# Kernel tuning notes

Hardware: AMD Instinct MI355X
Metric: run time of the kernel (lower is better)

## Reference

```python
import jax, jax.numpy as jnp
import numpy as np

N_E, N_R, E = 100000, 1000, 1000000
E_HID, R_HID = 128, 128
NEG_SLOPE = 0.01


def _seg_softmax(logits, seg, num_segments):
    # torch_geometric.utils.softmax: per-segment max-subtracted softmax, +1e-16 in denom
    m = jax.ops.segment_max(logits, seg, num_segments=num_segments)
    m = jnp.where(jnp.isfinite(m), m, 0.0)  # empty segments
    z = jnp.exp(logits - m[seg])
    s = jax.ops.segment_sum(z, seg, num_segments=num_segments)
    return z / (s[seg] + 1e-16)


def setup_inputs() -> dict:
    key = jax.random.key(0)
    ks = jax.random.split(key, 10)
    s_e = 1.0 / np.sqrt(E_HID)
    s_r = 1.0 / np.sqrt(R_HID)
    s_2r = 1.0 / np.sqrt(2 * R_HID)
    return {
        "x_e": jax.random.normal(ks[0], (N_E, E_HID), jnp.float32),
        "x_r": jax.random.normal(ks[1], (N_R, R_HID), jnp.float32),
        "edge_index": jax.random.randint(ks[2], (2, E), 0, N_E, jnp.int32),
        "rel": jax.random.randint(ks[3], (E,), 0, N_R, jnp.int32),
        "rel_all": jax.random.randint(ks[4], (N_R,), 0, N_R, jnp.int32),
        "w_ah": jax.random.uniform(ks[5], (E_HID,), jnp.float32, -s_e, s_e),
        "w_at": jax.random.uniform(ks[6], (E_HID,), jnp.float32, -s_e, s_e),
        "w_ar": jax.random.uniform(ks[7], (R_HID,), jnp.float32, -s_r, s_r),
        "W_r1": jax.random.uniform(ks[8], (R_HID, 2 * R_HID), jnp.float32, -s_r, s_r),
        "b_r1": jnp.zeros((2 * R_HID,), jnp.float32),
        "W_r2": jax.random.uniform(ks[9], (2 * R_HID, R_HID), jnp.float32, -s_2r, s_2r),
        "b_r2": jnp.zeros((R_HID,), jnp.float32),
        "W_r": jax.random.uniform(jax.random.fold_in(key, 99), (2 * R_HID, 2 * R_HID), jnp.float32, -s_2r, s_2r),
        "b_r": jnp.zeros((2 * R_HID,), jnp.float32),
    }


def reference(x_e, x_r, edge_index, rel, rel_all, w_ah, w_at, w_ar,
              W_r1, b_r1, W_r2, b_r2, W_r, b_r):
    h, t = edge_index[0], edge_index[1]
    n_e = x_e.shape[0]

    # per-node/per-rel attention scores, gathered per edge
    e_h = (x_e @ w_ah)[h]          # [E]
    e_t = (x_e @ w_at)[t]          # [E]
    e_r = (x_r @ w_ar)[rel]        # [E]

    alpha_h = _seg_softmax(jax.nn.leaky_relu(e_h + e_r, NEG_SLOPE), h, n_e)
    alpha_t = _seg_softmax(jax.nn.leaky_relu(e_t + e_r, NEG_SLOPE), t, n_e)

    # relation transform (no activation in original)
    x_r2 = (x_r @ W_r1 + b_r1) @ W_r2 + b_r2   # [N_r, r_hidden]
    msg = x_r + x_r2                            # [N_r, r_hidden]

    # sparse.mm(adj, msg) == weighted scatter-add over edges
    msg_e = msg[rel]                            # [E, r_hidden]
    x_e_h = jax.ops.segment_sum(alpha_h[:, None] * msg_e, h, num_segments=n_e)
    x_e_t = jax.ops.segment_sum(alpha_t[:, None] * msg_e, t, num_segments=n_e)

    x = jnp.concatenate([x_e_h, x_e_t], axis=1)  # [N_e, 2*r_hidden]
    return x @ W_r + b_r
```

## Files before the change

kernel.cpp:

```cpp
#include <hip/hip_runtime.h>
#include <hip/hip_fp16.h>


#define CH1    2048
#define SUPW   4096
#define CAP1   45056
#define CH2    4096
#define CHUNK2 (CAP1 / CH2)
#define NBPS   128
#define CAP2   512
#define MAXD   64
#define NSB    2048

#define MIX_LO(acc, w, z) \
    asm("v_fma_mix_f32 %0, %1, %2, %0 op_sel:[0,0,0] op_sel_hi:[1,0,0]" \
        : "+v"(acc) : "v"(w), "v"(z))
#define MIX_HI(acc, w, z) \
    asm("v_fma_mix_f32 %0, %1, %2, %0 op_sel:[1,0,0] op_sel_hi:[1,0,0]" \
        : "+v"(acc) : "v"(w), "v"(z))

__device__ __forceinline__ float dot4(float4 a, float4 b) {
    return a.x * b.x + a.y * b.y + a.z * b.z + a.w * b.w;
}

__global__ __launch_bounds__(256) void k_front(
    const float* __restrict__ xe, const float* __restrict__ xr,
    const float* __restrict__ wah, const float* __restrict__ wat, const float* __restrict__ war,
    const float* __restrict__ W1, const float* __restrict__ b1,
    const float* __restrict__ W2, const float* __restrict__ b2,
    const float* __restrict__ Wr,
    const int* __restrict__ ei,
    float* __restrict__ eh, float* __restrict__ et, float* __restrict__ er,
    __half* __restrict__ Mh, __half* __restrict__ Mt,
    int* __restrict__ hist,
    int nE, int nR, int E, int nH, int nSR) {
    __shared__ float xs[128];
    __shared__ float hs[256];
    __shared__ float ms[128];
    __shared__ int cnt[64];
    int b = blockIdx.x, tid = threadIdx.x;
    int lane = tid & 63;
    if (b < nR) {
        int r = b, j = tid;
        if (j < 128) xs[j] = xr[(size_t)r * 128 + j];
        __syncthreads();
        {
            float acc = b1[j];
            #pragma unroll 4
            for (int k = 0; k < 128; ++k) acc += xs[k] * W1[k * 256 + j];
            hs[j] = acc;
        }
        __syncthreads();
        if (j < 128) {
            float acc = b2[j] + xs[j];
            #pragma unroll 4
            for (int k = 0; k < 256; ++k) acc += hs[k] * W2[k * 128 + j];
            ms[j] = acc;
        }
        __syncthreads();
        {
            float ah = 0.f, at_ = 0.f;
            #pragma unroll 4
            for (int i = 0; i < 128; ++i) {
                float m = ms[i];
                ah  += m * Wr[i * 256 + j];
                at_ += m * Wr[(128 + i) * 256 + j];
            }
            Mh[(size_t)r * 256 + j] = __float2half(ah);
            Mt[(size_t)r * 256 + j] = __float2half(at_);
        }
    } else if (b < nR + nH) {
        int blk = b - nR;
        if (tid < 64) cnt[tid] = 0;
        __syncthreads();
        int base = blk * CH1;
        #pragma unroll
        for (int k = 0; k < CH1 / 256; ++k) {
            int e = base + k * 256 + tid;
            if (e < E) {
                unsigned vh = ((unsigned)ei[e]) << 1;
                unsigned vt = (((unsigned)ei[E + e]) << 1) | 1u;
                atomicAdd(&cnt[vh >> 12], 1);
                atomicAdd(&cnt[vt >> 12], 1);
            }
        }
        __syncthreads();
        if (tid < 64) hist[tid * 512 + blk] = cnt[tid];
    } else if (b < nR + nH + nSR) {
        int row = (b - nR - nH) * 32 + (tid >> 6) * 8 + (lane >> 3);
        int seg = lane & 7;
        if (row < nR) {
            const float4* xp = (const float4*)(xr + (size_t)row * 128 + seg * 16);
            const float4* cp = (const float4*)(war + seg * 16);
            float d = 0.f;
            #pragma unroll
            for (int q = 0; q < 4; ++q) d += dot4(xp[q], cp[q]);
            #pragma unroll
            for (int m = 4; m >= 1; m >>= 1) d += __shfl_xor(d, m);
            if (seg == 0) er[row] = d;
        }
    } else {
        int sb = b - nR - nH - nSR;
        int rowInTile = (tid >> 6) * 8 + (lane >> 3);
        int seg = lane & 7;
        const float4* ap = (const float4*)(wah + seg * 16);
        const float4* bp = (const float4*)(wat + seg * 16);
        float4 a0 = ap[0], a1 = ap[1], a2 = ap[2], a3 = ap[3];
        float4 b0 = bp[0], b1_ = bp[1], b2_ = bp[2], b3 = bp[3];
        int row0 = sb * 32 + rowInTile;
        int row1 = row0 + NSB * 32;
        int r1c = min(row1, nE - 1);
        const float4* p0 = (const float4*)(xe + (size_t)row0 * 128 + seg * 16);
        const float4* p1 = (const float4*)(xe + (size_t)r1c * 128 + seg * 16);
        float4 u0 = p0[0], u1 = p0[1], u2 = p0[2], u3 = p0[3];
        float4 w0 = p1[0], w1 = p1[1], w2 = p1[2], w3 = p1[3];
        float dh0 = dot4(u0, a0) + dot4(u1, a1) + dot4(u2, a2) + dot4(u3, a3);
        float dt0 = dot4(u0, b0) + dot4(u1, b1_) + dot4(u2, b2_) + dot4(u3, b3);
        float dh1 = dot4(w0, a0) + dot4(w1, a1) + dot4(w2, a2) + dot4(w3, a3);
        float dt1 = dot4(w0, b0) + dot4(w1, b1_) + dot4(w2, b2_) + dot4(w3, b3);
        #pragma unroll
        for (int m = 4; m >= 1; m >>= 1) {
            dh0 += __shfl_xor(dh0, m); dt0 += __shfl_xor(dt0, m);
            dh1 += __shfl_xor(dh1, m); dt1 += __shfl_xor(dt1, m);
        }
        if (seg == 0) {
            eh[row0] = dh0; et[row0] = dt0;
            if (row1 < nE) { eh[row1] = dh1; et[row1] = dt1; }
        }
    }
}

__global__ __launch_bounds__(256) void k_scanp(
    int* __restrict__ hist, int* __restrict__ bcur1,
    int* __restrict__ bcur2, int nbuck, int nblk) {
    __shared__ int wtot[4];
    int bin = blockIdx.x, tid = threadIdx.x, lane = tid & 63, wid = tid >> 6;
    for (int g = bin * 256 + tid; g < nbuck; g += 64 * 256) bcur2[g] = 0;
    int j0 = 2 * tid, j1 = 2 * tid + 1;
    int v0 = (j0 < nblk) ? hist[bin * 512 + j0] : 0;
    int v1 = (j1 < nblk) ? hist[bin * 512 + j1] : 0;
    int ts = v0 + v1;
    int incl = ts;
    #pragma unroll
    for (int d = 1; d < 64; d <<= 1) { int u = __shfl_up(incl, d); if (lane >= d) incl += u; }
    if (lane == 63) wtot[wid] = incl;
    __syncthreads();
    int wbase = 0;
    for (int w = 0; w < wid; ++w) wbase += wtot[w];
    int excl = wbase + incl - ts;
    hist[bin * 512 + j0] = excl;
    hist[bin * 512 + j1] = excl + v0;
    if (tid == 255) bcur1[bin] = wbase + incl;
}

__global__ __launch_bounds__(256) void k_part1(
    const int* __restrict__ ei, const int* __restrict__ rel,
    const int* __restrict__ hist, unsigned* __restrict__ part1, int E) {
    __shared__ unsigned stage[CH1 * 2];
    __shared__ int cnt[64], offs_[64], cur[64], gb[64];
    int tid = threadIdx.x;
    if (tid < 64) cnt[tid] = 0;
    __syncthreads();
    int base = blockIdx.x * CH1;
    unsigned wh[CH1 / 256], wt[CH1 / 256];
    bool ve[CH1 / 256];
    #pragma unroll
    for (int k = 0; k < CH1 / 256; ++k) {
        int e = base + k * 256 + tid;
        ve[k] = (e < E);
        unsigned h = 0, t = 0, r = 0;
        if (ve[k]) { h = (unsigned)ei[e]; t = (unsigned)ei[E + e]; r = (unsigned)rel[e]; }
        unsigned vh = h << 1, vt = (t << 1) | 1u;
        wh[k] = ((vh >> 12) << 26) | ((vh & 4095u) << 10) | r;
        wt[k] = ((vt >> 12) << 26) | ((vt & 4095u) << 10) | r;
        if (ve[k]) { atomicAdd(&cnt[wh[k] >> 26], 1); atomicAdd(&cnt[wt[k] >> 26], 1); }
    }
    __syncthreads();
    if (tid < 64) {
        int v = cnt[tid], incl = v;
        #pragma unroll
        for (int d = 1; d < 64; d <<= 1) { int u = __shfl_up(incl, d); if (tid >= d) incl += u; }
        offs_[tid] = incl - v;
        cur[tid] = incl - v;
        gb[tid] = hist[tid * 512 + blockIdx.x];
    }
    __syncthreads();
    #pragma unroll
    for (int k = 0; k < CH1 / 256; ++k) {
        if (ve[k]) {
            int p = atomicAdd(&cur[wh[k] >> 26], 1); stage[p] = wh[k];
            int q = atomicAdd(&cur[wt[k] >> 26], 1); stage[q] = wt[k];
        }
    }
    __syncthreads();
    int total = offs_[63] + cnt[63];
    for (int p = tid; p < total; p += 256) {
        unsigned w = stage[p];
        int bin = w >> 26;
        int dst = gb[bin] + (p - offs_[bin]);
        if (dst < CAP1) part1[(size_t)bin * CAP1 + dst] = w & 0x03FFFFFFu;
    }
}

__global__ __launch_bounds__(256) void k_part2(
    const int* __restrict__ bcur1, const unsigned* __restrict__ part1,
    int* __restrict__ bcur2, unsigned short* __restrict__ part2) {
    int s = blockIdx.x / CHUNK2, c = blockIdx.x % CHUNK2;
    int cnt_s = min(bcur1[s], CAP1);
    int start = c * CH2;
    if (start >= cnt_s) return;
    __shared__ unsigned stage[CH2];
    __shared__ int cnt[NBPS], offs_[NBPS], cur[NBPS], gb[NBPS];
    __shared__ int wt2[2];
    int tid = threadIdx.x;
    if (tid < NBPS) cnt[tid] = 0;
    __syncthreads();
    unsigned w_[CH2 / 256];
    bool v_[CH2 / 256];
    #pragma unroll
    for (int k = 0; k < CH2 / 256; ++k) {
        int i = start + k * 256 + tid;
        v_[k] = (i < cnt_s);
        unsigned it = v_[k] ? part1[(size_t)s * CAP1 + i] : 0u;
        unsigned sb = ((it >> 10) & 4095u) >> 5;
        unsigned entry = (((it >> 10) & 31u) << 10) | (it & 1023u);
        w_[k] = (sb << 16) | entry;
        if (v_[k]) atomicAdd(&cnt[sb], 1);
    }
    __syncthreads();
    int v128 = 0, incl128 = 0;
    if (tid < NBPS) {
        v128 = cnt[tid]; incl128 = v128;
        int lane = tid & 63;
        #pragma unroll
        for (int d = 1; d < 64; d <<= 1) { int u = __shfl_up(incl128, d); if (lane >= d) incl128 += u; }
        if (lane == 63) wt2[tid >> 6] = incl128;
    }
    __syncthreads();
    if (tid < NBPS) {
        int base2 = (tid >= 64) ? wt2[0] : 0;
        int excl = base2 + incl128 - v128;
        offs_[tid] = excl;
        cur[tid] = excl;
        gb[tid] = atomicAdd(&bcur2[s * NBPS + tid], v128);
    }
    __syncthreads();
    #pragma unroll
    for (int k = 0; k < CH2 / 256; ++k)
        if (v_[k]) { int p = atomicAdd(&cur[w_[k] >> 16], 1); stage[p] = w_[k]; }
    __syncthreads();
    int total = offs_[NBPS - 1] + cnt[NBPS - 1];
    for (int p = tid; p < total; p += 256) {
        unsigned w = stage[p];
        int sb = w >> 16;
        int dst = gb[sb] + (p - offs_[sb]);
        if (dst < CAP2) part2[((size_t)s * NBPS + sb) * CAP2 + dst] = (unsigned short)w;
    }
}

__global__ __launch_bounds__(256) void k_group_out10(
    const int* __restrict__ bcur2, const unsigned short* __restrict__ part2,
    const float* __restrict__ eh, const float* __restrict__ et, const float* __restrict__ er,
    const __half* __restrict__ Mh, const __half* __restrict__ Mt,
    const float* __restrict__ br, float* __restrict__ out, int nE, int nR) {
    __shared__ unsigned short csr[CAP2];
    __shared__ float er_s[1024];
    __shared__ unsigned zbufZ[4][2][64];
    __shared__ unsigned zbufO[4][2][64];
    __shared__ int cnt[32], offs_[32], cur[32];
    int b = blockIdx.x, tid = threadIdx.x;
    int count = min(bcur2[b], CAP2);
    unsigned mtOff = (unsigned)nR * 512u;
    if (tid < 32) cnt[tid] = 0;
    for (int i = tid; i < nR; i += 256) er_s[i] = er[i];
    __syncthreads();
    unsigned short ev[CAP2 / 256];
    bool val[CAP2 / 256];
    #pragma unroll
    for (int k = 0; k < CAP2 / 256; ++k) {
        int i = tid + k * 256;
        val[k] = (i < count);
        ev[k] = val[k] ? part2[(size_t)b * CAP2 + i] : (unsigned short)0;
        if (val[k]) atomicAdd(&cnt[ev[k] >> 10], 1);
    }
    __syncthreads();
    if (tid < 32) {
        int v = cnt[tid], incl = v;
        #pragma unroll
        for (int d = 1; d < 32; d <<= 1) { int u = __shfl_up(incl, d); if (tid >= d) incl += u; }
        offs_[tid] = incl - v;
        cur[tid] = incl - v;
    }
    __syncthreads();
    #pragma unroll
    for (int k = 0; k < CAP2 / 256; ++k) {
        if (val[k]) {
            int p = atomicAdd(&cur[ev[k] >> 10], 1);
            csr[p] = (unsigned short)(ev[k] & 1023u);
        }
    }
    __syncthreads();
    int lane = tid & 63, wid = tid >> 6;
    int half = lane >> 5, l31 = lane & 31;
    unsigned loff = (unsigned)(l31 << 4);
    const char* Mbase = (const char*)Mh;
    float4 bv = *(const float4*)(br + l31 * 8 + half * 4);
    int nbase = b * 16;
    for (int li = wid; li < 16; li += 4) {
        int n = nbase + li;
        if (n >= nE) break;
        int oH = offs_[2 * li];
        int oT = offs_[2 * li + 1];
        int dH = min(cur[2 * li] - oH, MAXD);
        int dT = min(cur[2 * li + 1] - oT, MAXD);
        float ehn = eh[n], etn = et[n];
        unsigned zHv = 0u, oHv = 0u;
        unsigned zTv = 0u, oTv = mtOff;
        if (lane < dH) {
            int r = csr[oH + lane];
            float l = ehn + er_s[r]; l = l > 0.f ? l : 0.01f * l;
            zHv = __float_as_uint(__expf(l)) & 0xFFFFFC00u;
            oHv = (unsigned)r << 9;
        }
        if (lane < dT) {
            int r = csr[oT + lane];
            float l = etn + er_s[r]; l = l > 0.f ? l : 0.01f * l;
            zTv = __float_as_uint(__expf(l)) & 0xFFFFFC00u;
            oTv = ((unsigned)r << 9) + mtOff;
        }
        zbufZ[wid][0][lane] = zHv; zbufO[wid][0][lane] = oHv;
        zbufZ[wid][1][lane] = zTv; zbufO[wid][1][lane] = oTv;
        const unsigned* zrowZ = &zbufZ[wid][half][0];
        const unsigned* zrowO = &zbufO[wid][half][0];
        float acc[8] = {0, 0, 0, 0, 0, 0, 0, 0};
        float s = 0.f;
        int kk = (max(dH, dT) + 3) & ~3;
        for (int j = 0; j < kk; j += 4) {
            uint4 z4 = *(const uint4*)(zrowZ + j);
            uint4 o4 = *(const uint4*)(zrowO + j);
            unsigned za[4] = {z4.x, z4.y, z4.z, z4.w};
            unsigned oa[4] = {o4.x, o4.y, o4.z, o4.w};
            #pragma unroll
            for (int i = 0; i < 4; ++i) {
                float z = __uint_as_float(za[i]);
                uint4 m = *(const uint4*)(Mbase + (oa[i] + loff));
                MIX_LO(acc[0], m.x, z); MIX_HI(acc[1], m.x, z);
                MIX_LO(acc[2], m.y, z); MIX_HI(acc[3], m.y, z);
                MIX_LO(acc[4], m.z, z); MIX_HI(acc[5], m.z, z);
                MIX_LO(acc[6], m.w, z); MIX_HI(acc[7], m.w, z);
                s += z;
            }
        }
        float sO = __shfl_xor(s, 32);
        float iMine = 1.f / (s + 1e-16f);
        float iOther = 1.f / (sO + 1e-16f);
        float oq[4];
        #pragma unroll
        for (int q = 0; q < 4; ++q) {
            float send = half ? acc[q] : acc[4 + q];
            float mine = half ? acc[4 + q] : acc[q];
            float recv = __shfl_xor(send, 32);
            oq[q] = mine * iMine + recv * iOther;
        }
        float4 o;
        o.x = oq[0] + bv.x;
        o.y = oq[1] + bv.y;
        o.z = oq[2] + bv.z;
        o.w = oq[3] + bv.w;
        *(float4*)(out + (size_t)n * 256 + l31 * 8 + half * 4) = o;
    }
}

__global__ __launch_bounds__(256) void k_scores(
    const float* __restrict__ xe, const float* __restrict__ xr,
    const float* __restrict__ wah, const float* __restrict__ wat, const float* __restrict__ war,
    float* __restrict__ eh, float* __restrict__ et, float* __restrict__ er,
    int nE, int nR) {
    int wid = (blockIdx.x * blockDim.x + threadIdx.x) >> 6;
    int lane = threadIdx.x & 63;
    if (wid < nE) {
        float2 x2 = *(const float2*)(xe + (size_t)wid * 128 + lane * 2);
        float2 a2 = *(const float2*)(wah + lane * 2);
        float2 b2 = *(const float2*)(wat + lane * 2);
        float dh = x2.x * a2.x + x2.y * a2.y;
        float dt = x2.x * b2.x + x2.y * b2.y;
        #pragma unroll
        for (int m = 32; m >= 1; m >>= 1) { dh += __shfl_xor(dh, m); dt += __shfl_xor(dt, m); }
        if (lane == 0) { eh[wid] = dh; et[wid] = dt; }
    } else if (wid < nE + nR) {
        int r = wid - nE;
        float2 x2 = *(const float2*)(xr + (size_t)r * 128 + lane * 2);
        float2 c2 = *(const float2*)(war + lane * 2);
        float d = x2.x * c2.x + x2.y * c2.y;
        #pragma unroll
        for (int m = 32; m >= 1; m >>= 1) d += __shfl_xor(d, m);
        if (lane == 0) er[r] = d;
    }
}

__global__ __launch_bounds__(256) void k_rel(
    const float* __restrict__ xr,
    const float* __restrict__ W1, const float* __restrict__ b1,
    const float* __restrict__ W2, const float* __restrict__ b2,
    const float* __restrict__ Wr,
    __half* __restrict__ Mh, __half* __restrict__ Mt) {
    __shared__ float xs[128];
    __shared__ float hs[256];
    __shared__ float ms[128];
    int r = blockIdx.x, j = threadIdx.x;
    if (j < 128) xs[j] = xr[(size_t)r * 128 + j];
    __syncthreads();
    {
        float acc = b1[j];
        #pragma unroll 4
        for (int k = 0; k < 128; ++k) acc += xs[k] * W1[k * 256 + j];
        hs[j] = acc;
    }
    __syncthreads();
    if (j < 128) {
        float acc = b2[j] + xs[j];
        #pragma unroll 4
        for (int k = 0; k < 256; ++k) acc += hs[k] * W2[k * 128 + j];
        ms[j] = acc;
    }
    __syncthreads();
    {
        float ah = 0.f, at_ = 0.f;
        #pragma unroll 4
        for (int i = 0; i < 128; ++i) {
            float m = ms[i];
            ah  += m * Wr[i * 256 + j];
            at_ += m * Wr[(128 + i) * 256 + j];
        }
        Mh[(size_t)r * 256 + j] = __float2half(ah);
        Mt[(size_t)r * 256 + j] = __float2half(at_);
    }
}

__global__ __launch_bounds__(256) void k_hist(
    const int* __restrict__ ei, int* __restrict__ deg, int E, int nE) {
    int e = blockIdx.x * blockDim.x + threadIdx.x;
    if (e >= E) return;
    atomicAdd(&deg[ei[e]], 1);
    atomicAdd(&deg[nE + ei[E + e]], 1);
}

__global__ __launch_bounds__(256) void k_scan1(
    const int* __restrict__ deg, int* __restrict__ offs, int* __restrict__ bsum, int N) {
    __shared__ int wtot[4];
    int tid = threadIdx.x, lane = tid & 63, wid = tid >> 6;
    int base = blockIdx.x * 1024 + tid * 4;
    int v[4];
    #pragma unroll
    for (int i = 0; i < 4; ++i) v[i] = (base + i < N) ? deg[base + i] : 0;
    int ts = v[0] + v[1] + v[2] + v[3];
    int incl = ts;
    #pragma unroll
    for (int d = 1; d < 64; d <<= 1) { int u = __shfl_up(incl, d); if (lane >= d) incl += u; }
    if (lane == 63) wtot[wid] = incl;
    __syncthreads();
    int wbase = 0;
    for (int w = 0; w < wid; ++w) wbase += wtot[w];
    int run = wbase + incl - ts;
    #pragma unroll
    for (int i = 0; i < 4; ++i) { if (base + i < N) offs[base + i] = run; run += v[i]; }
    if (tid == 255) bsum[blockIdx.x] = wbase + incl;
}

__global__ __launch_bounds__(256) void k_scan2(int* __restrict__ bsum, int NB) {
    __shared__ int wtot[4];
    int tid = threadIdx.x, lane = tid & 63, wid = tid >> 6;
    int v = (tid < NB) ? bsum[tid] : 0;
    int incl = v;
    #pragma unroll
    for (int d = 1; d < 64; d <<= 1) { int u = __shfl_up(incl, d); if (lane >= d) incl += u; }
    if (lane == 63) wtot[wid] = incl;
    __syncthreads();
    int wbase = 0;
    for (int w = 0; w < wid; ++w) wbase += wtot[w];
    if (tid < NB) bsum[tid] = wbase + incl - v;
}

__global__ __launch_bounds__(256) void k_scan3(
    int* __restrict__ offs, const int* __restrict__ bsum, int* __restrict__ cursor, int N) {
    int i = blockIdx.x * blockDim.x + threadIdx.x;
    if (i >= N) return;
    int v = offs[i] + bsum[i >> 10];
    offs[i] = v;
    cursor[i] = v;
}

__global__ __launch_bounds__(256) void k_scatter_offs(
    const int* __restrict__ ei, const int* __restrict__ rel,
    const float* __restrict__ eh, const float* __restrict__ et, const float* __restrict__ er,
    int* __restrict__ cursor, unsigned* __restrict__ csr, int E, int nE) {
    int e = blockIdx.x * blockDim.x + threadIdx.x;
    if (e >= E) return;
    int h = ei[e], t = ei[E + e], r = rel[e];
    float erv = er[r];
    float lh = eh[h] + erv; lh = lh > 0.f ? lh : 0.01f * lh;
    float lt = et[t] + erv; lt = lt > 0.f ? lt : 0.01f * lt;
    unsigned zh = (__float_as_uint(__expf(lh)) & 0xFFFFFC00u) | (unsigned)r;
    unsigned zt = (__float_as_uint(__expf(lt)) & 0xFFFFFC00u) | (unsigned)r;
    int ph = atomicAdd(&cursor[h], 1);
    csr[ph] = zh;
    int pt = atomicAdd(&cursor[nE + t], 1);
    csr[pt] = zt;
}

__global__ __launch_bounds__(256) void k_out_offs(
    const int* __restrict__ offs, const int* __restrict__ deg, const unsigned* __restrict__ csr,
    const __half* __restrict__ Mh, const __half* __restrict__ Mt, const float* __restrict__ br,
    float* __restrict__ out, int nE) {
    int wid = (blockIdx.x * blockDim.x + threadIdx.x) >> 6;
    int lane = threadIdx.x & 63;
    if (wid >= nE) return;
    int dH = deg[wid], dT = deg[nE + wid];
    size_t offH = (size_t)offs[wid], offT = (size_t)offs[nE + wid];
    float4 accH = {0, 0, 0, 0}, accT = {0, 0, 0, 0};
    float sH = 0.f, sT = 0.f;
    int dM = max(dH, dT);
    for (int b = 0; b < dM; b += 64) {
        int kH = min(64, dH - b);
        int kT = min(64, dT - b);
        unsigned eH = 0, eT = 0;
        if (lane < kH) eH = csr[offH + b + lane];
        if (lane < kT) eT = csr[offT + b + lane];
        int kk = max(kH, kT);
        for (int j = 0; j < kk; ++j) {
            unsigned cH = (unsigned)__shfl((int)eH, j);
            unsigned cT = (unsigned)__shfl((int)eT, j);
            if (j < kH) {
                float z = __uint_as_float(cH & 0xFFFFFC00u);
                int r = (int)(cH & 0x3FFu);
                const __half2* mp = (const __half2*)(Mh + ((size_t)r << 8) + (lane << 2));
                float2 m01 = __half22float2(mp[0]);
                float2 m23 = __half22float2(mp[1]);
                accH.x += z * m01.x; accH.y += z * m01.y;
                accH.z += z * m23.x; accH.w += z * m23.y;
                sH += z;
            }
            if (j < kT) {
                float z = __uint_as_float(cT & 0xFFFFFC00u);
                int r = (int)(cT & 0x3FFu);
                const __half2* mp = (const __half2*)(Mt + ((size_t)r << 8) + (lane << 2));
                float2 m01 = __half22float2(mp[0]);
                float2 m23 = __half22float2(mp[1]);
                accT.x += z * m01.x; accT.y += z * m01.y;
                accT.z += z * m23.x; accT.w += z * m23.y;
                sT += z;
            }
        }
    }
    float iH = 1.f / (sH + 1e-16f);
    float iT = 1.f / (sT + 1e-16f);
    float4 bv = *(const float4*)(br + lane * 4);
    float4 o;
    o.x = accH.x * iH + accT.x * iT + bv.x;
    o.y = accH.y * iH + accT.y * iT + bv.y;
    o.z = accH.z * iH + accT.z * iT + bv.z;
    o.w = accH.w * iH + accT.w * iT + bv.w;
    *(float4*)(out + (size_t)wid * 256 + lane * 4) = o;
}

extern "C" void kernel_launch(void* const* d_in, const int* in_sizes, int n_in,
                              void* d_out, int out_size, void* d_ws, size_t ws_size,
                              hipStream_t stream) {
    const float* xe  = (const float*)d_in[0];
    const float* xr  = (const float*)d_in[1];
    const int*   ei  = (const int*)d_in[2];
    const int*   rel = (const int*)d_in[3];
    const float* wah = (const float*)d_in[5];
    const float* wat = (const float*)d_in[6];
    const float* war = (const float*)d_in[7];
    const float* W1  = (const float*)d_in[8];
    const float* b1  = (const float*)d_in[9];
    const float* W2  = (const float*)d_in[10];
    const float* b2  = (const float*)d_in[11];
    const float* Wr  = (const float*)d_in[12];
    const float* br  = (const float*)d_in[13];
    float* out = (float*)d_out;

    const int nE = in_sizes[0] / 128;
    const int nR = in_sizes[1] / 128;
    const int E  = in_sizes[3];
    const int N  = 2 * nE;
    const int NSUP  = (N + SUPW - 1) / SUPW;
    const int NBUCK = NSUP * NBPS;
    const int NBLK1 = (E + CH1 - 1) / CH1;
    const int NSR   = (nR + 31) / 32;

    float* ws = (float*)d_ws;
    size_t o = 0;
    auto alloc = [&](size_t words) { size_t r = o; o += (words + 3) & ~(size_t)3; return r; };
    float* eh     = ws + alloc(nE);
    float* et     = ws + alloc(nE);
    float* er     = ws + alloc(nR);
    __half* Mh    = (__half*)(ws + alloc((size_t)nR * 128));
    __half* Mt    = (__half*)(ws + alloc((size_t)nR * 128));
    size_t common_words = o;

    size_t hist_words  = 64 * 512;
    size_t part1_words = (size_t)NSUP * CAP1;
    size_t part2_words = ((size_t)NBUCK * CAP2 + 1) / 2;
    size_t new_words = hist_words + 64 + NBUCK + part1_words + part2_words;
    bool planNew = (NBLK1 <= 512) && (NSUP <= 64) && (nE >= NSB * 32) &&
                   (ws_size >= (common_words + new_words + 64) * 4);

    if (planNew) {
        int* hist   = (int*)(ws + alloc(hist_words));
        int* bcur1  = (int*)(ws + alloc(64));
        int* bcur2  = (int*)(ws + alloc(NBUCK));
        unsigned* part1 = (unsigned*)(ws + alloc(part1_words));
        unsigned short* part2 = (unsigned short*)(ws + alloc(part2_words));
        k_front<<<nR + NBLK1 + NSR + NSB, 256, 0, stream>>>(
            xe, xr, wah, wat, war, W1, b1, W2, b2, Wr, ei,
            eh, et, er, Mh, Mt, hist, nE, nR, E, NBLK1, NSR);
        k_scanp<<<64, 256, 0, stream>>>(hist, bcur1, bcur2, NBUCK, NBLK1);
        k_part1<<<NBLK1, 256, 0, stream>>>(ei, rel, hist, part1, E);
        k_part2<<<NSUP * CHUNK2, 256, 0, stream>>>(bcur1, part1, bcur2, part2);
        k_group_out10<<<NBUCK, 256, 0, stream>>>(bcur2, part2, eh, et, er, Mh, Mt, br, out, nE, nR);
    } else {
        int* cursor = (int*)(ws + alloc(N));
        int* deg    = (int*)(ws + alloc(N));
        int* offs   = (int*)(ws + alloc(N));
        int* bsum   = (int*)(ws + alloc(512));
        unsigned* csr = (unsigned*)(ws + alloc(2 * (size_t)E));
        const int NB = (N + 1023) / 1024;
        k_scores<<<(nE + nR + 3) / 4, 256, 0, stream>>>(xe, xr, wah, wat, war, eh, et, er, nE, nR);
        k_rel<<<nR, 256, 0, stream>>>(xr, W1, b1, W2, b2, Wr, Mh, Mt);
        hipMemsetAsync(deg, 0, (size_t)N * sizeof(int), stream);
        k_hist<<<(E + 255) / 256, 256, 0, stream>>>(ei, deg, E, nE);
        k_scan1<<<NB, 256, 0, stream>>>(deg, offs, bsum, N);
        k_scan2<<<1, 256, 0, stream>>>(bsum, NB);
        k_scan3<<<(N + 255) / 256, 256, 0, stream>>>(offs, bsum, cursor, N);
        k_scatter_offs<<<(E + 255) / 256, 256, 0, stream>>>(ei, rel, eh, et, er, cursor, csr, E, nE);
        k_out_offs<<<(nE + 3) / 4, 256, 0, stream>>>(offs, deg, csr, Mh, Mt, br, out, nE);
    }
}
```

Before: 292.4 us.

## Tile relation MLP over 16 relations per block to reuse weight loads

The relation-transform branch of the fused front kernel now processes 16 relations per block instead of one. Each wave handles 4 relations, and each lane computes a vector of output columns, so every weight row loaded from W1, W2 and Wr is reused across 4 relations. The aim is to cut redundant weight traffic and the number of relation blocks by 16x. In exchange it uses more shared memory and registers per block and gives fewer, heavier blocks in this branch.

```diff
diff --git a/kernel.cpp b/kernel.cpp
--- a/kernel.cpp
+++ b/kernel.cpp
@@ -11,6 +11,7 @@
 #define CAP2   512
 #define MAXD   64
 #define NSB    2048
+#define RTILE  16
 
 #define MIX_LO(acc, w, z) \
     asm("v_fma_mix_f32 %0, %1, %2, %0 op_sel:[0,0,0] op_sel_hi:[1,0,0]" \
@@ -33,44 +34,100 @@
     float* __restrict__ eh, float* __restrict__ et, float* __restrict__ er,
     __half* __restrict__ Mh, __half* __restrict__ Mt,
     int* __restrict__ hist,
-    int nE, int nR, int E, int nH, int nSR) {
-    __shared__ float xs[128];
-    __shared__ float hs[256];
-    __shared__ float ms[128];
+    int nE, int nR, int E, int nRB, int nH, int nSR) {
+    __shared__ float xs2[RTILE][128];
+    __shared__ float hs2[RTILE][256];
     __shared__ int cnt[64];
     int b = blockIdx.x, tid = threadIdx.x;
     int lane = tid & 63;
-    if (b < nR) {
-        int r = b, j = tid;
-        if (j < 128) xs[j] = xr[(size_t)r * 128 + j];
+    if (b < nRB) {
+        int r0 = b * RTILE;
+        int w = tid >> 6;
+        for (int i = tid; i < RTILE * 128; i += 256) {
+            int rr = i >> 7, cc = i & 127;
+            int rg = min(r0 + rr, nR - 1);
+            xs2[rr][cc] = xr[(size_t)rg * 128 + cc];
+        }
         __syncthreads();
         {
-            float acc = b1[j];
+            float4 bb = *(const float4*)(b1 + lane * 4);
+            float4 acc0 = bb, acc1 = bb, acc2 = bb, acc3 = bb;
             #pragma unroll 4
-            for (int k = 0; k < 128; ++k) acc += xs[k] * W1[k * 256 + j];
-            hs[j] = acc;
-        }
-        __syncthreads();
-        if (j < 128) {
-            float acc = b2[j] + xs[j];
-            #pragma unroll 4
-            for (int k = 0; k < 256; ++k) acc += hs[k] * W2[k * 128 + j];
-            ms[j] = acc;
+            for (int k = 0; k < 128; ++k) {
+                float4 wv = *(const float4*)(W1 + k * 256 + lane * 4);
+                float x0 = xs2[w * 4 + 0][k], x1 = xs2[w * 4 + 1][k];
+                float x2 = xs2[w * 4 + 2][k], x3 = xs2[w * 4 + 3][k];
+                acc0.x += x0 * wv.x; acc0.y += x0 * wv.y; acc0.z += x0 * wv.z; acc0.w += x0 * wv.w;
+                acc1.x += x1 * wv.x; acc1.y += x1 * wv.y; acc1.z += x1 * wv.z; acc1.w += x1 * wv.w;
+                acc2.x += x2 * wv.x; acc2.y += x2 * wv.y; acc2.z += x2 * wv.z; acc2.w += x2 * wv.w;
+                acc3.x += x3 * wv.x; acc3.y += x3 * wv.y; acc3.z += x3 * wv.z; acc3.w += x3 * wv.w;
+            }
+            *(float4*)(&hs2[w * 4 + 0][lane * 4]) = acc0;
+            *(float4*)(&hs2[w * 4 + 1][lane * 4]) = acc1;
+            *(float4*)(&hs2[w * 4 + 2][lane * 4]) = acc2;
+            *(float4*)(&hs2[w * 4 + 3][lane * 4]) = acc3;
         }
         __syncthreads();
         {
-            float ah = 0.f, at_ = 0.f;
+            float2 bb = *(const float2*)(b2 + lane * 2);
+            float2 a0 = bb, a1 = bb, a2 = bb, a3 = bb;
             #pragma unroll 4
+            for (int k = 0; k < 256; ++k) {
+                float2 wv = *(const float2*)(W2 + k * 128 + lane * 2);
+                float h0 = hs2[w * 4 + 0][k], h1 = hs2[w * 4 + 1][k];
+                float h2 = hs2[w * 4 + 2][k], h3 = hs2[w * 4 + 3][k];
+                a0.x += h0 * wv.x; a0.y += h0 * wv.y;
+                a1.x += h1 * wv.x; a1.y += h1 * wv.y;
+                a2.x += h2 * wv.x; a2.y += h2 * wv.y;
+                a3.x += h3 * wv.x; a3.y += h3 * wv.y;
+            }
+            #pragma unroll
+            for (int r = 0; r < 4; ++r) {
+                int rr = w * 4 + r;
+                float2 acc = (r == 0) ? a0 : (r == 1) ? a1 : (r == 2) ? a2 : a3;
+                float2 xv = *(const float2*)(&xs2[rr][lane * 2]);
+                float2 mv; mv.x = acc.x + xv.x; mv.y = acc.y + xv.y;
+                *(float2*)(&xs2[rr][lane * 2]) = mv;
+            }
+        }
+        __syncthreads();
+        {
+            float4 h0 = {0,0,0,0}, h1 = {0,0,0,0}, h2 = {0,0,0,0}, h3 = {0,0,0,0};
+            float4 t0 = {0,0,0,0}, t1 = {0,0,0,0}, t2 = {0,0,0,0}, t3 = {0,0,0,0};
+            #pragma unroll 2
             for (int i = 0; i < 128; ++i) {
-                float m = ms[i];
-                ah  += m * Wr[i * 256 + j];
-                at_ += m * Wr[(128 + i) * 256 + j];
-            }
-            Mh[(size_t)r * 256 + j] = __float2half(ah);
-            Mt[(size_t)r * 256 + j] = __float2half(at_);
-        }
-    } else if (b < nR + nH) {
-        int blk = b - nR;
+                float4 wh = *(const float4*)(Wr + i * 256 + lane * 4);
+                float4 wt = *(const float4*)(Wr + (128 + i) * 256 + lane * 4);
+                float m0 = xs2[w * 4 + 0][i], m1 = xs2[w * 4 + 1][i];
+                float m2 = xs2[w * 4 + 2][i], m3 = xs2[w * 4 + 3][i];
+                h0.x += m0 * wh.x; h0.y += m0 * wh.y; h0.z += m0 * wh.z; h0.w += m0 * wh.w;
+                h1.x += m1 * wh.x; h1.y += m1 * wh.y; h1.z += m1 * wh.z; h1.w += m1 * wh.w;
+                h2.x += m2 * wh.x; h2.y += m2 * wh.y; h2.z += m2 * wh.z; h2.w += m2 * wh.w;
+                h3.x += m3 * wh.x; h3.y += m3 * wh.y; h3.z += m3 * wh.z; h3.w += m3 * wh.w;
+                t0.x += m0 * wt.x; t0.y += m0 * wt.y; t0.z += m0 * wt.z; t0.w += m0 * wt.w;
+                t1.x += m1 * wt.x; t1.y += m1 * wt.y; t1.z += m1 * wt.z; t1.w += m1 * wt.w;
+                t2.x += m2 * wt.x; t2.y += m2 * wt.y; t2.z += m2 * wt.z; t2.w += m2 * wt.w;
+                t3.x += m3 * wt.x; t3.y += m3 * wt.y; t3.z += m3 * wt.z; t3.w += m3 * wt.w;
+            }
+            #pragma unroll
+            for (int r = 0; r < 4; ++r) {
+                int rg = r0 + w * 4 + r;
+                if (rg < nR) {
+                    float4 ah = (r == 0) ? h0 : (r == 1) ? h1 : (r == 2) ? h2 : h3;
+                    float4 at_ = (r == 0) ? t0 : (r == 1) ? t1 : (r == 2) ? t2 : t3;
+                    __half2 p0 = __floats2half2_rn(ah.x, ah.y);
+                    __half2 p1 = __floats2half2_rn(ah.z, ah.w);
+                    __half2 q0 = __floats2half2_rn(at_.x, at_.y);
+                    __half2 q1 = __floats2half2_rn(at_.z, at_.w);
+                    *(__half2*)(Mh + (size_t)rg * 256 + lane * 4) = p0;
+                    *(__half2*)(Mh + (size_t)rg * 256 + lane * 4 + 2) = p1;
+                    *(__half2*)(Mt + (size_t)rg * 256 + lane * 4) = q0;
+                    *(__half2*)(Mt + (size_t)rg * 256 + lane * 4 + 2) = q1;
+                }
+            }
+        }
+    } else if (b < nRB + nH) {
+        int blk = b - nRB;
         if (tid < 64) cnt[tid] = 0;
         __syncthreads();
         int base = blk * CH1;
@@ -86,8 +143,8 @@
         }
         __syncthreads();
         if (tid < 64) hist[tid * 512 + blk] = cnt[tid];
-    } else if (b < nR + nH + nSR) {
-        int row = (b - nR - nH) * 32 + (tid >> 6) * 8 + (lane >> 3);
+    } else if (b < nRB + nH + nSR) {
+        int row = (b - nRB - nH) * 32 + (tid >> 6) * 8 + (lane >> 3);
         int seg = lane & 7;
         if (row < nR) {
             const float4* xp = (const float4*)(xr + (size_t)row * 128 + seg * 16);
@@ -100,7 +157,7 @@
             if (seg == 0) er[row] = d;
         }
     } else {
-        int sb = b - nR - nH - nSR;
+        int sb = b - nRB - nH - nSR;
         int rowInTile = (tid >> 6) * 8 + (lane >> 3);
         int seg = lane & 7;
         const float4* ap = (const float4*)(wah + seg * 16);
@@ -589,6 +646,7 @@
     const int NBUCK = NSUP * NBPS;
     const int NBLK1 = (E + CH1 - 1) / CH1;
     const int NSR   = (nR + 31) / 32;
+    const int NRB   = (nR + RTILE - 1) / RTILE;
 
     float* ws = (float*)d_ws;
     size_t o = 0;
@@ -613,9 +671,9 @@
         int* bcur2  = (int*)(ws + alloc(NBUCK));
         unsigned* part1 = (unsigned*)(ws + alloc(part1_words));
         unsigned short* part2 = (unsigned short*)(ws + alloc(part2_words));
-        k_front<<<nR + NBLK1 + NSR + NSB, 256, 0, stream>>>(
+        k_front<<<NRB + NBLK1 + NSR + NSB, 256, 0, stream>>>(
             xe, xr, wah, wat, war, W1, b1, W2, b2, Wr, ei,
-            eh, et, er, Mh, Mt, hist, nE, nR, E, NBLK1, NSR);
+            eh, et, er, Mh, Mt, hist, nE, nR, E, NRB, NBLK1, NSR);
         k_scanp<<<64, 256, 0, stream>>>(hist, bcur1, bcur2, NBUCK, NBLK1);
         k_part1<<<NBLK1, 256, 0, stream>>>(ei, rel, hist, part1, E);
         k_part2<<<NSUP * CHUNK2, 256, 0, stream>>>(bcur1, part1, bcur2, part2);
```

Result: slower. 315.8 us (+8.0%).
